# Kernel optimization log

Hardware: AMD Instinct MI355X
Metric: run time of the kernel (lower is better)

The kernel has to match this reference:

```python
import jax, jax.numpy as jnp
import numpy as np
import math

BS, S, D_IN, D_OUT, RANK = 4, 2048, 4096, 4096, 128
BASE_LR = 0.01
EPS = 1e-6
SQRT_IN = math.sqrt(D_IN)  # scalar_scaler


def setup_inputs() -> dict:
    key = jax.random.key(0)
    ks = jax.random.split(key, 8)
    return {
        "x": jax.random.normal(ks[0], (BS, S, D_IN), dtype=jnp.float32),
        "log_lr": jax.random.normal(ks[1], (RANK, D_IN), dtype=jnp.float32) * 0.01,
        "state": jax.random.normal(ks[2], (BS, RANK, D_IN), dtype=jnp.float32) * 0.02,
        "grad_buffer": jax.random.normal(ks[3], (BS, RANK, D_IN), dtype=jnp.float32) * 0.01,
        "w_bsp": jax.random.normal(ks[4], (RANK, D_IN), dtype=jnp.float32) * 0.02,
        "w_out": jax.random.normal(ks[5], (D_OUT, RANK), dtype=jnp.float32) * 0.02,
        "w_lin": jax.random.normal(ks[6], (D_OUT, D_IN), dtype=jnp.float32) * 0.02,
        "b_lin": jnp.zeros((D_OUT,), dtype=jnp.float32),
    }


def reference(x, log_lr, state, grad_buffer, w_bsp, w_out, w_lin, b_lin):
    # lr = base_lr * exp(log_lr * sqrt(in_features))  -> [rank, in]
    lr = BASE_LR * jnp.exp(log_lr * SQRT_IN)
    # s = lr[None] * state  -> [bs, rank, in]; state is detached in the original
    s = lr[None] * state
    # z = einsum('boi,bsi->bso', s, x)  -> [bs, seq, rank]
    z = jnp.einsum("bri,bsi->bsr", s, x)
    # FoItttFunction.apply is identity on z in the forward
    # z + base_state_proj(x)
    z = z + jnp.einsum("bsi,ri->bsr", x, w_bsp)
    # out_proj(z) + linear(x)
    y = jnp.einsum("bsr,or->bso", z, w_out) + jnp.einsum("bsi,oi->bso", x, w_lin) + b_lin
    return y
```

## Files before the change

kernel.cpp:

```cpp
#include <hip/hip_runtime.h>
#include <hip/hip_bf16.h>

typedef __attribute__((ext_vector_type(8))) short bf16x8;
typedef __attribute__((ext_vector_type(4))) float f32x4;

#define DEVI static __device__ __forceinline__

constexpr int BS = 4, SEQ = 2048, DIN = 4096, DOUT = 4096, RANK = 128;
constexpr int MTOT = BS * SEQ;

DEVI unsigned short f2bf(float f) {
  __hip_bfloat16 h = __float2bfloat16(f);
  return __builtin_bit_cast(unsigned short, h);
}


__global__ void cast_bf16_kernel(const float* __restrict__ src,
                                 unsigned short* __restrict__ dst, int n4) {
  int i = blockIdx.x * blockDim.x + threadIdx.x;
  int stride = gridDim.x * blockDim.x;
  for (; i < n4; i += stride) {
    float4 v = reinterpret_cast<const float4*>(src)[i];
    ushort4 o;
    o.x = f2bf(v.x); o.y = f2bf(v.y); o.z = f2bf(v.z); o.w = f2bf(v.w);
    reinterpret_cast<ushort4*>(dst)[i] = o;
  }
}

__global__ void prep_m_kernel(const float* __restrict__ log_lr,
                              const float* __restrict__ state,
                              const float* __restrict__ w_bsp,
                              unsigned short* __restrict__ m_bf) {
  const int n4 = BS * RANK * DIN / 4;
  int i = blockIdx.x * blockDim.x + threadIdx.x;
  int stride = gridDim.x * blockDim.x;
  for (; i < n4; i += stride) {
    int ri4 = (i * 4) % (RANK * DIN) / 4;
    float4 ll = reinterpret_cast<const float4*>(log_lr)[ri4];
    float4 wb = reinterpret_cast<const float4*>(w_bsp)[ri4];
    float4 st = reinterpret_cast<const float4*>(state)[i];
    ushort4 o;
    o.x = f2bf(0.01f * __expf(ll.x * 64.0f) * st.x + wb.x);
    o.y = f2bf(0.01f * __expf(ll.y * 64.0f) * st.y + wb.y);
    o.z = f2bf(0.01f * __expf(ll.z * 64.0f) * st.z + wb.z);
    o.w = f2bf(0.01f * __expf(ll.w * 64.0f) * st.w + wb.w);
    reinterpret_cast<ushort4*>(m_bf)[i] = o;
  }
}


DEVI void gload16(const void* g, void* l) {
  __builtin_amdgcn_global_load_lds(
      (const __attribute__((address_space(1))) void*)g,
      (__attribute__((address_space(3))) void*)l, 16, 0, 0);
}

template <int ROWS>
DEVI void stage_tile(const char* gbase, int ldBytes, char* lds) {
  const int lane = threadIdx.x & 63;
  const int wave = threadIdx.x >> 6;
  constexpr int CHUNKS = ROWS / 16;
  constexpr int CPW = CHUNKS / 4;
  const int colByte = (lane & 3) << 4;
  const int rowInChunk = lane >> 2;
#pragma unroll
  for (int c = 0; c < CPW; ++c) {
    int chunk = wave * CPW + c;
    int row = chunk * 16 + rowInChunk;
    gload16(gbase + (size_t)row * ldBytes + colByte, lds + chunk * 1024);
  }
}

template <int F>
DEVI void compute_tile(const char* lA, const char* lB, f32x4 (&acc)[F][F]) {
  const int lane = threadIdx.x & 63;
  const int wave = threadIdx.x >> 6;
  const int wr = wave >> 1, wc = wave & 1;
  const int kByte = (lane >> 4) * 16;
  const int rsel = lane & 15;
  bf16x8 a[F], b[F];
#pragma unroll
  for (int mi = 0; mi < F; ++mi) {
    int row = wr * (F * 16) + mi * 16 + rsel;
    a[mi] = *reinterpret_cast<const bf16x8*>(lA + row * 64 + kByte);
  }
#pragma unroll
  for (int ni = 0; ni < F; ++ni) {
    int row = wc * (F * 16) + ni * 16 + rsel;
    b[ni] = *reinterpret_cast<const bf16x8*>(lB + row * 64 + kByte);
  }
#pragma unroll
  for (int mi = 0; mi < F; ++mi)
#pragma unroll
    for (int ni = 0; ni < F; ++ni)
      acc[mi][ni] =
          __builtin_amdgcn_mfma_f32_16x16x32_bf16(a[mi], b[ni], acc[mi][ni], 0, 0, 0);
}

template <int KS>
__global__ __launch_bounds__(256) void z_gemm_splitk(
    const unsigned short* __restrict__ xbf, const unsigned short* __restrict__ mbf,
    float* __restrict__ zpart) {
  int bid = blockIdx.x;
  int ksl = bid & (KS - 1);
  int rest = bid / KS;
  int nt = rest & 1, mt = rest >> 1;
  int row0 = mt * 64;
  int batch = row0 >> 11;
  int kbase = ksl * (DIN / KS);
  const char* xb = (const char*)(xbf + (size_t)row0 * DIN + kbase);
  const char* mb = (const char*)(mbf + ((size_t)batch * RANK + nt * 64) * DIN + kbase);
  __shared__ __align__(16) char lA[2][64 * 64];
  __shared__ __align__(16) char lB[2][64 * 64];
  f32x4 acc[2][2] = {};
  constexpr int NT = DIN / KS / 32;
  stage_tile<64>(xb, DIN * 2, lA[0]);
  stage_tile<64>(mb, DIN * 2, lB[0]);
  for (int t = 0; t < NT; ++t) {
    __syncthreads();
    if (t + 1 < NT) {
      stage_tile<64>(xb + (t + 1) * 64, DIN * 2, lA[(t + 1) & 1]);
      stage_tile<64>(mb + (t + 1) * 64, DIN * 2, lB[(t + 1) & 1]);
    }
    compute_tile<2>(lA[t & 1], lB[t & 1], acc);
  }
  const int lane = threadIdx.x & 63;
  const int wave = threadIdx.x >> 6;
  const int wr = wave >> 1, wc = wave & 1;
#pragma unroll
  for (int mi = 0; mi < 2; ++mi)
#pragma unroll
    for (int ni = 0; ni < 2; ++ni) {
      int c = nt * 64 + wc * 32 + ni * 16 + (lane & 15);
      int r0 = row0 + wr * 32 + mi * 16 + (lane >> 4) * 4;
#pragma unroll
      for (int j = 0; j < 4; ++j)
        zpart[((size_t)ksl * MTOT + r0 + j) * RANK + c] = acc[mi][ni][j];
    }
}

template <int KS>
__global__ void z_reduce_kernel(const float* __restrict__ zpart,
                                unsigned short* __restrict__ zbf) {
  const int n4 = MTOT * RANK / 4;
  int i = blockIdx.x * blockDim.x + threadIdx.x;
  if (i >= n4) return;
  float4 s = reinterpret_cast<const float4*>(zpart)[i];
#pragma unroll
  for (int k = 1; k < KS; ++k) {
    float4 v = reinterpret_cast<const float4*>(zpart)[(size_t)k * n4 + i];
    s.x += v.x; s.y += v.y; s.z += v.z; s.w += v.w;
  }
  ushort4 o;
  o.x = f2bf(s.x); o.y = f2bf(s.y); o.z = f2bf(s.z); o.w = f2bf(s.w);
  reinterpret_cast<ushort4*>(zbf)[i] = o;
}

__global__ __launch_bounds__(256) void z_gemm_kernel(
    const unsigned short* __restrict__ xbf, const unsigned short* __restrict__ mbf,
    unsigned short* __restrict__ zbf) {
  int mt = blockIdx.x >> 1, nt = blockIdx.x & 1;
  int row0 = mt * 64;
  int batch = row0 >> 11;
  const char* xb = (const char*)(xbf + (size_t)row0 * DIN);
  const char* mb = (const char*)(mbf + ((size_t)batch * RANK + nt * 64) * DIN);
  __shared__ __align__(16) char lA[2][64 * 64];
  __shared__ __align__(16) char lB[2][64 * 64];
  f32x4 acc[2][2] = {};
  constexpr int NT = DIN / 32;
  stage_tile<64>(xb, DIN * 2, lA[0]);
  stage_tile<64>(mb, DIN * 2, lB[0]);
  for (int t = 0; t < NT; ++t) {
    __syncthreads();
    if (t + 1 < NT) {
      stage_tile<64>(xb + (t + 1) * 64, DIN * 2, lA[(t + 1) & 1]);
      stage_tile<64>(mb + (t + 1) * 64, DIN * 2, lB[(t + 1) & 1]);
    }
    compute_tile<2>(lA[t & 1], lB[t & 1], acc);
  }
  const int lane = threadIdx.x & 63;
  const int wave = threadIdx.x >> 6;
  const int wr = wave >> 1, wc = wave & 1;
#pragma unroll
  for (int mi = 0; mi < 2; ++mi)
#pragma unroll
    for (int ni = 0; ni < 2; ++ni) {
      int c = nt * 64 + wc * 32 + ni * 16 + (lane & 15);
      int r0 = row0 + wr * 32 + mi * 16 + (lane >> 4) * 4;
#pragma unroll
      for (int j = 0; j < 4; ++j)
        zbf[(size_t)(r0 + j) * RANK + c] = f2bf(acc[mi][ni][j]);
    }
}


struct MainCtx {
  const char* lds;
  int wr, wc, rsel, kgrp, xorv;
};

DEVI const bf16x8* lda_frag(const MainCtx& c, int d, int mi, int ks) {
  int col = ((ks * 64) + c.kgrp * 16) ^ c.xorv;
  return reinterpret_cast<const bf16x8*>(
      c.lds + d * 32768 + c.wr * 16384 + mi * 2048 + c.rsel * 128 + col);
}
DEVI const bf16x8* ldb_frag(const MainCtx& c, int d, int ni, int ks) {
  int col = ((ks * 64) + c.kgrp * 16) ^ c.xorv;
  return reinterpret_cast<const bf16x8*>(
      c.lds + 65536 + d * 32768 + (c.wc >> 1) * 16384 + (c.wc & 1) * 8192 +
      ni * 2048 + c.rsel * 128 + col);
}

template <int PH>
struct PhaseCfg {
  static constexpr int q = PH & 3;
  static constexpr int mih = q & 1;
  static constexpr int aCur = PH & 1;
  static constexpr int aNxt = (PH + 1) & 1;
  static constexpr int bCur = (PH >> 1) & 1;
  static constexpr int nq = (PH + 1) & 3;
  static constexpr int nbuf = ((PH + 1) >> 2) & 1;
  static constexpr int nks = nq >> 1;
  static constexpr int nmih = nq & 1;
  static constexpr bool rdB = (PH & 1) == 1;
  static constexpr int bNxt = ((PH + 1) >> 1) & 1;
};

template <int PH, bool VM0, class STG>
DEVI void phase(const MainCtx& c, f32x4 (&acc)[8][4], bf16x8 (&aS)[2][4],
                bf16x8 (&bS)[2][4], STG&& stg) {
  using P = PhaseCfg<PH>;
#pragma unroll
  for (int m = 0; m < 4; ++m)
    aS[P::aNxt][m] = *lda_frag(c, P::nbuf, P::nmih * 4 + m, P::nks);
  if constexpr (P::rdB) {
#pragma unroll
    for (int ni = 0; ni < 4; ++ni)
      bS[P::bNxt][ni] = *ldb_frag(c, P::nbuf, ni, P::nks);
  }
  stg();
  __builtin_amdgcn_s_setprio(1);
#pragma unroll
  for (int m = 0; m < 4; ++m)
#pragma unroll
    for (int ni = 0; ni < 4; ++ni)
      acc[P::mih * 4 + m][ni] = __builtin_amdgcn_mfma_f32_16x16x32_bf16(
          aS[P::aCur][m], bS[P::bCur][ni], acc[P::mih * 4 + m][ni], 0, 0, 0);
  __builtin_amdgcn_s_setprio(0);
  if constexpr (VM0)
    asm volatile("s_waitcnt vmcnt(0)" ::: "memory");
  else
    asm volatile("" ::: "memory");
  __builtin_amdgcn_s_barrier();
}

__global__ __launch_bounds__(512, 2) void main_gemm_8p(
    const unsigned short* __restrict__ xbf, const unsigned short* __restrict__ wlbf,
    const unsigned short* __restrict__ zbf, const unsigned short* __restrict__ wobf,
    const float* __restrict__ b_lin, float* __restrict__ out) {
  __shared__ __align__(16) char lds[131072];

  const int tid = threadIdx.x;
  const int lane = tid & 63, wave = tid >> 6;

  int bid = blockIdx.x;
  int swz = (bid & 7) * 64 + (bid >> 3);
  int mt = swz >> 4, nt = swz & 15;
  const int row0 = mt * 256, col0 = nt * 256;

  const char* xb = (const char*)(xbf + (size_t)row0 * DIN);
  const char* wb = (const char*)(wlbf + (size_t)col0 * DIN);
  const char* zb = (const char*)(zbf + (size_t)row0 * RANK);
  const char* ob = (const char*)(wobf + (size_t)col0 * RANK);

  const int srow8 = lane >> 3;
  const int scolS = ((lane & 7) ^ srow8) << 4;
  const int chunk0 = wave * 2;

  auto stage = [&](const char* gbase, int ld, int ldsOff) {
    gload16(gbase + (size_t)(chunk0 * 8 + srow8) * ld + scolS,
            (void*)&lds[ldsOff + chunk0 * 1024]);
    gload16(gbase + (size_t)(chunk0 * 8 + 8 + srow8) * ld + scolS,
            (void*)&lds[ldsOff + chunk0 * 1024 + 1024]);
  };
  auto stageA = [&](int k, int h, int d) {
    const char* g; int ld;
    if (k < 64) { g = xb + (size_t)h * 128 * (DIN * 2) + (size_t)k * 128; ld = DIN * 2; }
    else        { g = zb + (size_t)h * 128 * (RANK * 2) + (size_t)(k - 64) * 128; ld = RANK * 2; }
    stage(g, ld, d * 32768 + h * 16384);
  };
  auto stageB = [&](int k, int h, int d) {
    const char* g; int ld;
    if (k < 64) { g = wb + (size_t)h * 128 * (DIN * 2) + (size_t)k * 128; ld = DIN * 2; }
    else        { g = ob + (size_t)h * 128 * (RANK * 2) + (size_t)(k - 64) * 128; ld = RANK * 2; }
    stage(g, ld, 65536 + d * 32768 + h * 16384);
  };

  MainCtx c{lds, wave >> 2, wave & 3, lane & 15, lane >> 4, (lane & 7) << 4};

  f32x4 acc[8][4] = {};
  bf16x8 aS[2][4], bS[2][4];

  stageA(0, 0, 0); stageA(0, 1, 0);
  stageB(0, 0, 0); stageB(0, 1, 0);
  stageB(1, 0, 1);
  asm volatile("s_waitcnt vmcnt(2)" ::: "memory");
  __builtin_amdgcn_s_barrier();
#pragma unroll
  for (int m = 0; m < 4; ++m) aS[0][m] = *lda_frag(c, 0, m, 0);
#pragma unroll
  for (int ni = 0; ni < 4; ++ni) bS[0][ni] = *ldb_frag(c, 0, ni, 0);

  constexpr int NKT = 66;
  for (int j = 0; j < NKT / 2; ++j) {
    int t = 2 * j;
    int kA1 = (t + 1 < NKT - 1) ? t + 1 : NKT - 1;
    int kN2 = (t + 2 < NKT - 1) ? t + 2 : NKT - 1;
    int kB3 = (t + 3 < NKT - 1) ? t + 3 : NKT - 1;
    phase<0, false>(c, acc, aS, bS,
                    [&] { stageA(kA1, 0, 1); stageA(kA1, 1, 1); stageB(kA1, 1, 1); });
    phase<1, false>(c, acc, aS, bS, [&] {});
    phase<2, true >(c, acc, aS, bS, [&] {});
    phase<3, false>(c, acc, aS, bS, [&] { stageB(kN2, 0, 0); });
    phase<4, false>(c, acc, aS, bS,
                    [&] { stageA(kN2, 0, 0); stageA(kN2, 1, 0); stageB(kN2, 1, 0); });
    phase<5, false>(c, acc, aS, bS, [&] {});
    phase<6, true >(c, acc, aS, bS, [&] {});
    phase<7, false>(c, acc, aS, bS, [&] { stageB(kB3, 0, 1); });
  }
  asm volatile("s_waitcnt vmcnt(0)" ::: "memory");

  const int wr = wave >> 2, wc = wave & 3;
  const int rbase = row0 + wr * 128 + (lane >> 4) * 4;
  const int cbase = col0 + wc * 64 + (lane & 15);
#pragma unroll
  for (int mi = 0; mi < 8; ++mi)
#pragma unroll
    for (int ni = 0; ni < 4; ++ni) {
      int cc = cbase + ni * 16;
      float bv = b_lin[cc];
      int r = rbase + mi * 16;
#pragma unroll
      for (int j2 = 0; j2 < 4; ++j2)
        out[(size_t)(r + j2) * DOUT + cc] = acc[mi][ni][j2] + bv;
    }
}


extern "C" void kernel_launch(void* const* d_in, const int* in_sizes, int n_in,
                              void* d_out, int out_size, void* d_ws, size_t ws_size,
                              hipStream_t stream) {
  const float* x = (const float*)d_in[0];
  const float* log_lr = (const float*)d_in[1];
  const float* state = (const float*)d_in[2];
  const float* w_bsp = (const float*)d_in[4];
  const float* w_out = (const float*)d_in[5];
  const float* w_lin = (const float*)d_in[6];
  const float* b_lin = (const float*)d_in[7];
  float* out = (float*)d_out;

  unsigned short* xbf = (unsigned short*)d_ws;
  unsigned short* wlbf = xbf + (size_t)MTOT * DIN;
  unsigned short* wobf = wlbf + (size_t)DOUT * DIN;
  unsigned short* mbf = wobf + (size_t)DOUT * RANK;
  unsigned short* zbf = mbf + (size_t)BS * RANK * DIN;
  float* zpart = (float*)(zbf + (size_t)MTOT * RANK);
  const size_t need_split = 108003328 + 16777216;

  cast_bf16_kernel<<<2048, 256, 0, stream>>>(x, xbf, MTOT * DIN / 4);
  cast_bf16_kernel<<<2048, 256, 0, stream>>>(w_lin, wlbf, DOUT * DIN / 4);
  cast_bf16_kernel<<<512, 256, 0, stream>>>(w_out, wobf, DOUT * RANK / 4);
  prep_m_kernel<<<2048, 256, 0, stream>>>(log_lr, state, w_bsp, mbf);

  if (ws_size >= need_split) {
    z_gemm_splitk<4><<<1024, 256, 0, stream>>>(xbf, mbf, zpart);
    z_reduce_kernel<4><<<1024, 256, 0, stream>>>(zpart, zbf);
  } else {
    z_gemm_kernel<<<256, 256, 0, stream>>>(xbf, mbf, zbf);
  }

  main_gemm_8p<<<512, 512, 0, stream>>>(xbf, wlbf, zbf, wobf, b_lin, out);
}
```

Measured before the change: 554.4 us.

## Switch main GEMM to 32x32x16 MFMA and fuse prep kernels into one launch

The main GEMM moves from 16x16x32 to 32x32x16 bf16 MFMA tiles. Each wave now holds 4x2 f32x16 accumulators, and the LDS fragment addressing, phase schedule and epilogue are rebuilt to match. Both A and B tiles are now staged together once per buffer swap, and the prologue waits for all loads to finish. The four cast/prep kernels are merged into one grid-stride kernel to cut launch overhead. The larger MFMA tile reduces the number of LDS fragment reads per FLOP, at the cost of a less overlapped prologue and a different B-staging pipeline.

```diff
diff --git a/kernel.cpp b/kernel.cpp
--- a/kernel.cpp
+++ b/kernel.cpp
@@ -3,6 +3,7 @@
 
 typedef __attribute__((ext_vector_type(8))) short bf16x8;
 typedef __attribute__((ext_vector_type(4))) float f32x4;
+typedef __attribute__((ext_vector_type(16))) float f32x16;
 
 #define DEVI static __device__ __forceinline__
 
@@ -15,36 +16,51 @@
 }
 
 
-__global__ void cast_bf16_kernel(const float* __restrict__ src,
-                                 unsigned short* __restrict__ dst, int n4) {
+__global__ void prep_all_kernel(const float* __restrict__ x,
+                                const float* __restrict__ w_lin,
+                                const float* __restrict__ w_out,
+                                const float* __restrict__ log_lr,
+                                const float* __restrict__ state,
+                                const float* __restrict__ w_bsp,
+                                unsigned short* __restrict__ xbf,
+                                unsigned short* __restrict__ wlbf,
+                                unsigned short* __restrict__ wobf,
+                                unsigned short* __restrict__ mbf) {
+  constexpr int N_X = MTOT * DIN / 4;
+  constexpr int N_WL = DOUT * DIN / 4;
+  constexpr int N_WO = DOUT * RANK / 4;
+  constexpr int N_M = BS * RANK * DIN / 4;
+  constexpr int O1 = N_X, O2 = O1 + N_WL, O3 = O2 + N_WO, O4 = O3 + N_M;
   int i = blockIdx.x * blockDim.x + threadIdx.x;
   int stride = gridDim.x * blockDim.x;
-  for (; i < n4; i += stride) {
-    float4 v = reinterpret_cast<const float4*>(src)[i];
-    ushort4 o;
-    o.x = f2bf(v.x); o.y = f2bf(v.y); o.z = f2bf(v.z); o.w = f2bf(v.w);
-    reinterpret_cast<ushort4*>(dst)[i] = o;
-  }
-}
-
-__global__ void prep_m_kernel(const float* __restrict__ log_lr,
-                              const float* __restrict__ state,
-                              const float* __restrict__ w_bsp,
-                              unsigned short* __restrict__ m_bf) {
-  const int n4 = BS * RANK * DIN / 4;
-  int i = blockIdx.x * blockDim.x + threadIdx.x;
-  int stride = gridDim.x * blockDim.x;
-  for (; i < n4; i += stride) {
-    int ri4 = (i * 4) % (RANK * DIN) / 4;
-    float4 ll = reinterpret_cast<const float4*>(log_lr)[ri4];
-    float4 wb = reinterpret_cast<const float4*>(w_bsp)[ri4];
-    float4 st = reinterpret_cast<const float4*>(state)[i];
-    ushort4 o;
-    o.x = f2bf(0.01f * __expf(ll.x * 64.0f) * st.x + wb.x);
-    o.y = f2bf(0.01f * __expf(ll.y * 64.0f) * st.y + wb.y);
-    o.z = f2bf(0.01f * __expf(ll.z * 64.0f) * st.z + wb.z);
-    o.w = f2bf(0.01f * __expf(ll.w * 64.0f) * st.w + wb.w);
-    reinterpret_cast<ushort4*>(m_bf)[i] = o;
+  for (; i < O4; i += stride) {
+    if (i < O1) {
+      float4 v = reinterpret_cast<const float4*>(x)[i];
+      ushort4 o{f2bf(v.x), f2bf(v.y), f2bf(v.z), f2bf(v.w)};
+      reinterpret_cast<ushort4*>(xbf)[i] = o;
+    } else if (i < O2) {
+      int j = i - O1;
+      float4 v = reinterpret_cast<const float4*>(w_lin)[j];
+      ushort4 o{f2bf(v.x), f2bf(v.y), f2bf(v.z), f2bf(v.w)};
+      reinterpret_cast<ushort4*>(wlbf)[j] = o;
+    } else if (i < O3) {
+      int j = i - O2;
+      float4 v = reinterpret_cast<const float4*>(w_out)[j];
+      ushort4 o{f2bf(v.x), f2bf(v.y), f2bf(v.z), f2bf(v.w)};
+      reinterpret_cast<ushort4*>(wobf)[j] = o;
+    } else {
+      int j = i - O3;
+      int ri4 = j & (RANK * DIN / 4 - 1);
+      float4 ll = reinterpret_cast<const float4*>(log_lr)[ri4];
+      float4 wb = reinterpret_cast<const float4*>(w_bsp)[ri4];
+      float4 st = reinterpret_cast<const float4*>(state)[j];
+      ushort4 o;
+      o.x = f2bf(0.01f * __expf(ll.x * 64.0f) * st.x + wb.x);
+      o.y = f2bf(0.01f * __expf(ll.y * 64.0f) * st.y + wb.y);
+      o.z = f2bf(0.01f * __expf(ll.z * 64.0f) * st.z + wb.z);
+      o.w = f2bf(0.01f * __expf(ll.w * 64.0f) * st.w + wb.w);
+      reinterpret_cast<ushort4*>(mbf)[j] = o;
+    }
   }
 }
 
@@ -195,57 +211,58 @@
 
 
 struct MainCtx {
-  const char* lds;
-  int wr, wc, rsel, kgrp, xorv;
+  const char* aBase;
+  const char* bBase;
+  int hi16;
+  int xorv;
 };
 
-DEVI const bf16x8* lda_frag(const MainCtx& c, int d, int mi, int ks) {
-  int col = ((ks * 64) + c.kgrp * 16) ^ c.xorv;
-  return reinterpret_cast<const bf16x8*>(
-      c.lds + d * 32768 + c.wr * 16384 + mi * 2048 + c.rsel * 128 + col);
-}
-DEVI const bf16x8* ldb_frag(const MainCtx& c, int d, int ni, int ks) {
-  int col = ((ks * 64) + c.kgrp * 16) ^ c.xorv;
-  return reinterpret_cast<const bf16x8*>(
-      c.lds + 65536 + d * 32768 + (c.wc >> 1) * 16384 + (c.wc & 1) * 8192 +
-      ni * 2048 + c.rsel * 128 + col);
-}
-
-template <int PH>
-struct PhaseCfg {
-  static constexpr int q = PH & 3;
-  static constexpr int mih = q & 1;
-  static constexpr int aCur = PH & 1;
-  static constexpr int aNxt = (PH + 1) & 1;
-  static constexpr int bCur = (PH >> 1) & 1;
-  static constexpr int nq = (PH + 1) & 3;
-  static constexpr int nbuf = ((PH + 1) >> 2) & 1;
-  static constexpr int nks = nq >> 1;
-  static constexpr int nmih = nq & 1;
-  static constexpr bool rdB = (PH & 1) == 1;
-  static constexpr int bNxt = ((PH + 1) >> 1) & 1;
+DEVI const bf16x8* lda32(const MainCtx& c, int d, int rf, int ks) {
+  int col = (ks * 32 + c.hi16) ^ c.xorv;
+  return reinterpret_cast<const bf16x8*>(c.aBase + d * 32768 + rf * 4096 + col);
+}
+DEVI const bf16x8* ldb32(const MainCtx& c, int d, int cf, int ks) {
+  int col = (ks * 32 + c.hi16) ^ c.xorv;
+  return reinterpret_cast<const bf16x8*>(c.bBase + d * 32768 + cf * 4096 + col);
+}
+
+template <int P>
+struct PC {
+  static constexpr int q = P & 3;
+  static constexpr int kp = q >> 1, cf = q & 1;
+  static constexpr int aCur = (P >> 1) & 1;
+  static constexpr int bCur = P & 1;
+  static constexpr int nP = (P + 1) & 7;
+  static constexpr int nq = nP & 3;
+  static constexpr int nbuf = nP >> 2;
+  static constexpr int nkp = nq >> 1, ncf = nq & 1;
+  static constexpr bool rdA = (ncf == 0);
+  static constexpr int aNxt = (nP >> 1) & 1;
+  static constexpr int bNxt = nP & 1;
 };
 
-template <int PH, bool VM0, class STG>
-DEVI void phase(const MainCtx& c, f32x4 (&acc)[8][4], bf16x8 (&aS)[2][4],
-                bf16x8 (&bS)[2][4], STG&& stg) {
-  using P = PhaseCfg<PH>;
-#pragma unroll
-  for (int m = 0; m < 4; ++m)
-    aS[P::aNxt][m] = *lda_frag(c, P::nbuf, P::nmih * 4 + m, P::nks);
-  if constexpr (P::rdB) {
-#pragma unroll
-    for (int ni = 0; ni < 4; ++ni)
-      bS[P::bNxt][ni] = *ldb_frag(c, P::nbuf, ni, P::nks);
-  }
+template <int P, bool VM0, class STG>
+DEVI void phase32(const MainCtx& c, f32x16 (&acc)[4][2], bf16x8 (&aS)[2][8],
+                  bf16x8 (&bS)[2][2], STG&& stg) {
+  using K = PC<P>;
+  if constexpr (K::rdA) {
+#pragma unroll
+    for (int rf = 0; rf < 4; ++rf)
+#pragma unroll
+      for (int kk = 0; kk < 2; ++kk)
+        aS[K::aNxt][rf * 2 + kk] = *lda32(c, K::nbuf, rf, K::nkp * 2 + kk);
+  }
+#pragma unroll
+  for (int kk = 0; kk < 2; ++kk)
+    bS[K::bNxt][kk] = *ldb32(c, K::nbuf, K::ncf, K::nkp * 2 + kk);
   stg();
   __builtin_amdgcn_s_setprio(1);
 #pragma unroll
-  for (int m = 0; m < 4; ++m)
-#pragma unroll
-    for (int ni = 0; ni < 4; ++ni)
-      acc[P::mih * 4 + m][ni] = __builtin_amdgcn_mfma_f32_16x16x32_bf16(
-          aS[P::aCur][m], bS[P::bCur][ni], acc[P::mih * 4 + m][ni], 0, 0, 0);
+  for (int kk = 0; kk < 2; ++kk)
+#pragma unroll
+    for (int rf = 0; rf < 4; ++rf)
+      acc[rf][K::cf] = __builtin_amdgcn_mfma_f32_32x32x16_bf16(
+          aS[K::aCur][rf * 2 + kk], bS[K::bCur][kk], acc[rf][K::cf], 0, 0, 0);
   __builtin_amdgcn_s_setprio(0);
   if constexpr (VM0)
     asm volatile("s_waitcnt vmcnt(0)" ::: "memory");
@@ -254,7 +271,7 @@
   __builtin_amdgcn_s_barrier();
 }
 
-__global__ __launch_bounds__(512, 2) void main_gemm_8p(
+__global__ __launch_bounds__(512, 2) void main_gemm_32(
     const unsigned short* __restrict__ xbf, const unsigned short* __restrict__ wlbf,
     const unsigned short* __restrict__ zbf, const unsigned short* __restrict__ wobf,
     const float* __restrict__ b_lin, float* __restrict__ out) {
@@ -262,6 +279,7 @@
 
   const int tid = threadIdx.x;
   const int lane = tid & 63, wave = tid >> 6;
+  const int wr = wave >> 2, wc = wave & 3;
 
   int bid = blockIdx.x;
   int swz = (bid & 7) * 64 + (bid >> 3);
@@ -296,53 +314,59 @@
     stage(g, ld, 65536 + d * 32768 + h * 16384);
   };
 
-  MainCtx c{lds, wave >> 2, wave & 3, lane & 15, lane >> 4, (lane & 7) << 4};
-
-  f32x4 acc[8][4] = {};
-  bf16x8 aS[2][4], bS[2][4];
+  MainCtx c{lds + wr * 16384 + (lane & 31) * 128,
+            lds + 65536 + (wc >> 1) * 16384 + (wc & 1) * 8192 + (lane & 31) * 128,
+            (lane >> 5) * 16, (lane & 7) << 4};
+
+  f32x16 acc[4][2] = {};
+  bf16x8 aS[2][8], bS[2][2];
 
   stageA(0, 0, 0); stageA(0, 1, 0);
   stageB(0, 0, 0); stageB(0, 1, 0);
-  stageB(1, 0, 1);
-  asm volatile("s_waitcnt vmcnt(2)" ::: "memory");
+  asm volatile("s_waitcnt vmcnt(0)" ::: "memory");
   __builtin_amdgcn_s_barrier();
 #pragma unroll
-  for (int m = 0; m < 4; ++m) aS[0][m] = *lda_frag(c, 0, m, 0);
-#pragma unroll
-  for (int ni = 0; ni < 4; ++ni) bS[0][ni] = *ldb_frag(c, 0, ni, 0);
+  for (int rf = 0; rf < 4; ++rf)
+#pragma unroll
+    for (int kk = 0; kk < 2; ++kk)
+      aS[0][rf * 2 + kk] = *lda32(c, 0, rf, kk);
+#pragma unroll
+  for (int kk = 0; kk < 2; ++kk) bS[0][kk] = *ldb32(c, 0, 0, kk);
 
   constexpr int NKT = 66;
   for (int j = 0; j < NKT / 2; ++j) {
     int t = 2 * j;
-    int kA1 = (t + 1 < NKT - 1) ? t + 1 : NKT - 1;
-    int kN2 = (t + 2 < NKT - 1) ? t + 2 : NKT - 1;
-    int kB3 = (t + 3 < NKT - 1) ? t + 3 : NKT - 1;
-    phase<0, false>(c, acc, aS, bS,
-                    [&] { stageA(kA1, 0, 1); stageA(kA1, 1, 1); stageB(kA1, 1, 1); });
-    phase<1, false>(c, acc, aS, bS, [&] {});
-    phase<2, true >(c, acc, aS, bS, [&] {});
-    phase<3, false>(c, acc, aS, bS, [&] { stageB(kN2, 0, 0); });
-    phase<4, false>(c, acc, aS, bS,
-                    [&] { stageA(kN2, 0, 0); stageA(kN2, 1, 0); stageB(kN2, 1, 0); });
-    phase<5, false>(c, acc, aS, bS, [&] {});
-    phase<6, true >(c, acc, aS, bS, [&] {});
-    phase<7, false>(c, acc, aS, bS, [&] { stageB(kB3, 0, 1); });
+    int k1 = (t + 1 < NKT - 1) ? t + 1 : NKT - 1;
+    int k2 = (t + 2 < NKT - 1) ? t + 2 : NKT - 1;
+    phase32<0, false>(c, acc, aS, bS, [&] {
+      stageA(k1, 0, 1); stageA(k1, 1, 1); stageB(k1, 0, 1); stageB(k1, 1, 1);
+    });
+    phase32<1, false>(c, acc, aS, bS, [&] {});
+    phase32<2, true >(c, acc, aS, bS, [&] {});
+    phase32<3, false>(c, acc, aS, bS, [&] {});
+    phase32<4, false>(c, acc, aS, bS, [&] {
+      stageA(k2, 0, 0); stageA(k2, 1, 0); stageB(k2, 0, 0); stageB(k2, 1, 0);
+    });
+    phase32<5, false>(c, acc, aS, bS, [&] {});
+    phase32<6, true >(c, acc, aS, bS, [&] {});
+    phase32<7, false>(c, acc, aS, bS, [&] {});
   }
   asm volatile("s_waitcnt vmcnt(0)" ::: "memory");
 
-  const int wr = wave >> 2, wc = wave & 3;
-  const int rbase = row0 + wr * 128 + (lane >> 4) * 4;
-  const int cbase = col0 + wc * 64 + (lane & 15);
-#pragma unroll
-  for (int mi = 0; mi < 8; ++mi)
-#pragma unroll
-    for (int ni = 0; ni < 4; ++ni) {
-      int cc = cbase + ni * 16;
+  const int rbase0 = row0 + wr * 128 + (lane >> 5) * 4;
+  const int cbase0 = col0 + wc * 64 + (lane & 31);
+#pragma unroll
+  for (int rf = 0; rf < 4; ++rf)
+#pragma unroll
+    for (int cf = 0; cf < 2; ++cf) {
+      int cc = cbase0 + cf * 32;
       float bv = b_lin[cc];
-      int r = rbase + mi * 16;
-#pragma unroll
-      for (int j2 = 0; j2 < 4; ++j2)
-        out[(size_t)(r + j2) * DOUT + cc] = acc[mi][ni][j2] + bv;
+      int rb = rbase0 + rf * 32;
+#pragma unroll
+      for (int reg = 0; reg < 16; ++reg) {
+        int r = rb + (reg & 3) + 8 * (reg >> 2);
+        out[(size_t)r * DOUT + cc] = acc[rf][cf][reg] + bv;
+      }
     }
 }
 
@@ -367,10 +391,8 @@
   float* zpart = (float*)(zbf + (size_t)MTOT * RANK);
   const size_t need_split = 108003328 + 16777216;
 
-  cast_bf16_kernel<<<2048, 256, 0, stream>>>(x, xbf, MTOT * DIN / 4);
-  cast_bf16_kernel<<<2048, 256, 0, stream>>>(w_lin, wlbf, DOUT * DIN / 4);
-  cast_bf16_kernel<<<512, 256, 0, stream>>>(w_out, wobf, DOUT * RANK / 4);
-  prep_m_kernel<<<2048, 256, 0, stream>>>(log_lr, state, w_bsp, mbf);
+  prep_all_kernel<<<2048, 256, 0, stream>>>(x, w_lin, w_out, log_lr, state, w_bsp,
+                                            xbf, wlbf, wobf, mbf);
 
   if (ws_size >= need_split) {
     z_gemm_splitk<4><<<1024, 256, 0, stream>>>(xbf, mbf, zpart);
@@ -379,5 +401,5 @@
     z_gemm_kernel<<<256, 256, 0, stream>>>(xbf, mbf, zbf);
   }
 
-  main_gemm_8p<<<512, 512, 0, stream>>>(xbf, wlbf, zbf, wobf, b_lin, out);
-}
+  main_gemm_32<<<512, 512, 0, stream>>>(xbf, wlbf, zbf, wobf, b_lin, out);
+}
```

Result: slower. 578.8 us (+4.4%).
